# Kernel optimization log

Hardware: AMD Instinct MI355X
Metric: run time of the kernel (lower is better)

The kernel has to match this reference:

```python
import jax, jax.numpy as jnp
import numpy as np

EPS = 1e-12  # torch F.normalize default eps

def _l1_normalize(x):
    # F.normalize(x, p=1, dim=1): divide by channel-wise L1 norm, clamped at eps
    n = jnp.sum(jnp.abs(x), axis=1, keepdims=True)
    return x / jnp.maximum(n, EPS)

def setup_inputs() -> dict:
    key = jax.random.key(0)
    k1, k2, k3 = jax.random.split(key, 3)
    shape = (2, 128, 64, 64)  # B, C, H, W
    return {
        "a": jax.random.normal(k1, shape, dtype=jnp.float32),
        "b": jax.random.normal(k2, shape, dtype=jnp.float32),
        "c": jax.random.normal(k3, shape, dtype=jnp.float32),
    }

def reference(a, b, c):
    a = _l1_normalize(a)
    b = _l1_normalize(b)
    c = _l1_normalize(c)
    sim_ab = jnp.einsum('bchw,bcij->bhwij', a, b)
    sim_ac = jnp.einsum('bchw,bcij->bhwij', a, c)
    # F.l1_loss default reduction='mean'
    return jnp.mean(jnp.abs(sim_ac - sim_ab))
```

## Files before the change

### kernel.cpp

```cpp
#include <hip/hip_runtime.h>
#include <stdint.h>

#define HW 4096
#define NC 128
#define BATCH 2

typedef __attribute__((ext_vector_type(8))) short bf16x8;
typedef __attribute__((ext_vector_type(4))) float f32x4;
typedef __attribute__((ext_vector_type(8))) unsigned short u16x8;

__device__ __forceinline__ unsigned short f32_to_bf16(float f) {
    union { float f; unsigned int u; } v; v.f = f;
    unsigned int u = v.u;
    unsigned int r = (u + 0x7FFFu + ((u >> 16) & 1u)) >> 16;
    return (unsigned short)r;
}

__device__ __forceinline__ void async_cp16(const void* g, void* s) {
    __builtin_amdgcn_global_load_lds(
        (const __attribute__((address_space(1))) uint32_t*)g,
        (__attribute__((address_space(3))) uint32_t*)s, 16, 0, 0);
}

__global__ __launch_bounds__(512) void norm_kernel(
    const float* __restrict__ A, const float* __restrict__ B,
    const float* __restrict__ Cc,
    unsigned short* __restrict__ anT, unsigned short* __restrict__ dT,
    float* __restrict__ out) {
    const int tid = threadIdx.x;
    if (blockIdx.x == 0 && tid == 0) *out = 0.f;
    const int pl = tid & 31;
    const int cg = tid >> 5;
    const int gp = blockIdx.x * 32;
    const int bb = gp >> 12;
    const int p  = (gp & (HW - 1)) + pl;
    const size_t base = (size_t)bb * NC * HW + p;
    const int c0 = cg * 8;

    float va[8], vb[8], vc[8];
    float sa = 0.f, sb = 0.f, sc = 0.f;
#pragma unroll
    for (int k = 0; k < 8; ++k) {
        size_t idx = base + (size_t)(c0 + k) * HW;
        va[k] = A[idx]; vb[k] = B[idx]; vc[k] = Cc[idx];
        sa += fabsf(va[k]); sb += fabsf(vb[k]); sc += fabsf(vc[k]);
    }
    __shared__ float red[3][16][32];
    red[0][cg][pl] = sa; red[1][cg][pl] = sb; red[2][cg][pl] = sc;
    __syncthreads();
    float na = 0.f, nb = 0.f, nc = 0.f;
#pragma unroll
    for (int g = 0; g < 16; ++g) {
        na += red[0][g][pl]; nb += red[1][g][pl]; nc += red[2][g][pl];
    }
    const float ra = 1.f / fmaxf(na, 1e-12f);
    const float rb = 1.f / fmaxf(nb, 1e-12f);
    const float rc = 1.f / fmaxf(nc, 1e-12f);

    const size_t obase = ((size_t)bb * HW + p) * NC;
    const int slot = cg ^ (p & 15);
    u16x8 xa, xd;
#pragma unroll
    for (int j = 0; j < 8; ++j) {
        xa[j] = f32_to_bf16(va[j] * ra);
        xd[j] = f32_to_bf16(vc[j] * rc - vb[j] * rb);
    }
    *(u16x8*)(anT + obase + slot * 8) = xa;
    *(u16x8*)(dT  + obase + slot * 8) = xd;
}

__global__ __launch_bounds__(256, 2) void simloss_kernel(
    const unsigned short* __restrict__ anT, const unsigned short* __restrict__ dT,
    float* __restrict__ out) {
    __shared__ uint4 smem4[4096];
    const int tid = threadIdx.x;
    const int b   = blockIdx.x;
    const int bz  = b >> 8;
    const int my  = (b & 255) >> 3;
    const int ng  = b & 7;
    const char* gA = (const char*)(anT + ((size_t)bz * HW + my * 128) * NC);
    const char* gB0 = (const char*)(dT + ((size_t)bz * HW + ng * 4 * 128) * NC);

    const int wv  = tid >> 6;
    const int ln  = tid & 63;
    char* sA = (char*)smem4;
    char* sB = (char*)(smem4 + 2048);

#pragma unroll
    for (int i = 0; i < 8; ++i) {
        const size_t goff = (size_t)(i * 256 + tid) * 16;
        const size_t loff = (size_t)i * 4096 + wv * 1024;
        async_cp16(gA + goff, sA + loff);
        async_cp16(gB0 + goff, sB + loff);
    }
    __syncthreads();

    const int m16  = ln & 15;
    const int quad = ln >> 4;
    const int wr   = (wv >> 1) * 64;
    const int wc   = (wv & 1) * 64;

    float s = 0.f;
    for (int j = 0; j < 4; ++j) {
        f32x4 acc[4][4] = {};
#pragma unroll
        for (int ks = 0; ks < 4; ++ks) {
            const int chunk = ks * 4 + quad;
            const int slot  = chunk ^ m16;
            bf16x8 af[4], bfr[4];
#pragma unroll
            for (int mi = 0; mi < 4; ++mi)
                af[mi] = *(const bf16x8*)(sA + (wr + mi * 16 + m16) * 256 + slot * 16);
#pragma unroll
            for (int ni = 0; ni < 4; ++ni)
                bfr[ni] = *(const bf16x8*)(sB + (wc + ni * 16 + m16) * 256 + slot * 16);
#pragma unroll
            for (int mi = 0; mi < 4; ++mi)
#pragma unroll
                for (int ni = 0; ni < 4; ++ni)
                    acc[mi][ni] = __builtin_amdgcn_mfma_f32_16x16x32_bf16(
                        af[mi], bfr[ni], acc[mi][ni], 0, 0, 0);
        }
#pragma unroll
        for (int mi = 0; mi < 4; ++mi)
#pragma unroll
            for (int ni = 0; ni < 4; ++ni)
#pragma unroll
                for (int r = 0; r < 4; ++r)
                    s += fabsf(acc[mi][ni][r]);

        __syncthreads();
        if (j < 3) {
            const char* gBn = gB0 + (size_t)(j + 1) * 32768;
#pragma unroll
            for (int i = 0; i < 8; ++i) {
                const size_t goff = (size_t)(i * 256 + tid) * 16;
                const size_t loff = (size_t)i * 4096 + wv * 1024;
                async_cp16(gBn + goff, sB + loff);
            }
            __syncthreads();
        }
    }

#pragma unroll
    for (int off = 32; off > 0; off >>= 1)
        s += __shfl_down(s, off);
    if (ln == 0) ((float*)smem4)[wv] = s;
    __syncthreads();
    if (tid == 0) {
        const float inv = 1.0f / ((float)BATCH * (float)HW * (float)HW);
        float t = ((float*)smem4)[0] + ((float*)smem4)[1] +
                  ((float*)smem4)[2] + ((float*)smem4)[3];
        atomicAdd(out, t * inv);
    }
}

extern "C" void kernel_launch(void* const* d_in, const int* in_sizes, int n_in,
                              void* d_out, int out_size, void* d_ws, size_t ws_size,
                              hipStream_t stream) {
    const float* A  = (const float*)d_in[0];
    const float* B  = (const float*)d_in[1];
    const float* Cc = (const float*)d_in[2];
    float* out = (float*)d_out;
    unsigned short* anT = (unsigned short*)d_ws;
    unsigned short* dT  = anT + (size_t)BATCH * HW * NC;

    norm_kernel<<<dim3(256), dim3(512), 0, stream>>>(A, B, Cc, anT, dT, out);
    simloss_kernel<<<dim3(512), dim3(256), 0, stream>>>(anT, dT, out);
}
```

Before: 79.90 us.

## Keep A fragments in registers and double-buffer B tiles in LDS

The similarity kernel now loads its A-tile MFMA fragments into registers once. That frees the A region of shared memory to act as a second B buffer, so the next B tile's async global-to-LDS copy runs while the current tile is being computed, and one barrier per iteration is removed. The normalization kernel is also reshaped so each thread handles two pixels with float2 loads, using 256 threads per block instead of 512. The cost is higher register pressure from the 64 VGPRs of A fragments, which could limit occupancy under the existing launch bounds.

After: 80.73 us. No clear change (+1.0%).

```diff
diff --git a/kernel.cpp b/kernel.cpp
--- a/kernel.cpp
+++ b/kernel.cpp
@@ -22,51 +22,65 @@
         (__attribute__((address_space(3))) uint32_t*)s, 16, 0, 0);
 }
 
-__global__ __launch_bounds__(512) void norm_kernel(
+__global__ __launch_bounds__(256) void norm_kernel(
     const float* __restrict__ A, const float* __restrict__ B,
     const float* __restrict__ Cc,
     unsigned short* __restrict__ anT, unsigned short* __restrict__ dT,
     float* __restrict__ out) {
     const int tid = threadIdx.x;
     if (blockIdx.x == 0 && tid == 0) *out = 0.f;
-    const int pl = tid & 31;
-    const int cg = tid >> 5;
+    const int pl = tid & 15;
+    const int cg = tid >> 4;
     const int gp = blockIdx.x * 32;
     const int bb = gp >> 12;
-    const int p  = (gp & (HW - 1)) + pl;
-    const size_t base = (size_t)bb * NC * HW + p;
+    const int p0 = (gp & (HW - 1)) + pl * 2;
+    const size_t base = (size_t)bb * NC * HW + p0;
     const int c0 = cg * 8;
 
-    float va[8], vb[8], vc[8];
-    float sa = 0.f, sb = 0.f, sc = 0.f;
+    float2 va[8], vb[8], vc[8];
+    float sa0 = 0.f, sa1 = 0.f, sb0 = 0.f, sb1 = 0.f, sc0 = 0.f, sc1 = 0.f;
 #pragma unroll
     for (int k = 0; k < 8; ++k) {
         size_t idx = base + (size_t)(c0 + k) * HW;
-        va[k] = A[idx]; vb[k] = B[idx]; vc[k] = Cc[idx];
-        sa += fabsf(va[k]); sb += fabsf(vb[k]); sc += fabsf(vc[k]);
+        va[k] = *(const float2*)(A + idx);
+        vb[k] = *(const float2*)(B + idx);
+        vc[k] = *(const float2*)(Cc + idx);
+        sa0 += fabsf(va[k].x); sa1 += fabsf(va[k].y);
+        sb0 += fabsf(vb[k].x); sb1 += fabsf(vb[k].y);
+        sc0 += fabsf(vc[k].x); sc1 += fabsf(vc[k].y);
     }
     __shared__ float red[3][16][32];
-    red[0][cg][pl] = sa; red[1][cg][pl] = sb; red[2][cg][pl] = sc;
+    red[0][cg][pl * 2] = sa0; red[0][cg][pl * 2 + 1] = sa1;
+    red[1][cg][pl * 2] = sb0; red[1][cg][pl * 2 + 1] = sb1;
+    red[2][cg][pl * 2] = sc0; red[2][cg][pl * 2 + 1] = sc1;
     __syncthreads();
-    float na = 0.f, nb = 0.f, nc = 0.f;
+    float na0 = 0.f, na1 = 0.f, nb0 = 0.f, nb1 = 0.f, nc0 = 0.f, nc1 = 0.f;
 #pragma unroll
     for (int g = 0; g < 16; ++g) {
-        na += red[0][g][pl]; nb += red[1][g][pl]; nc += red[2][g][pl];
+        na0 += red[0][g][pl * 2]; na1 += red[0][g][pl * 2 + 1];
+        nb0 += red[1][g][pl * 2]; nb1 += red[1][g][pl * 2 + 1];
+        nc0 += red[2][g][pl * 2]; nc1 += red[2][g][pl * 2 + 1];
     }
-    const float ra = 1.f / fmaxf(na, 1e-12f);
-    const float rb = 1.f / fmaxf(nb, 1e-12f);
-    const float rc = 1.f / fmaxf(nc, 1e-12f);
+    const float ra0 = 1.f / fmaxf(na0, 1e-12f), ra1 = 1.f / fmaxf(na1, 1e-12f);
+    const float rb0 = 1.f / fmaxf(nb0, 1e-12f), rb1 = 1.f / fmaxf(nb1, 1e-12f);
+    const float rc0 = 1.f / fmaxf(nc0, 1e-12f), rc1 = 1.f / fmaxf(nc1, 1e-12f);
 
-    const size_t obase = ((size_t)bb * HW + p) * NC;
-    const int slot = cg ^ (p & 15);
-    u16x8 xa, xd;
+    const size_t ob0 = ((size_t)bb * HW + p0) * NC;
+    const size_t ob1 = ob0 + NC;
+    const int sl0 = cg ^ (p0 & 15);
+    const int sl1 = cg ^ ((p0 + 1) & 15);
+    u16x8 xa0, xa1, xd0, xd1;
 #pragma unroll
     for (int j = 0; j < 8; ++j) {
-        xa[j] = f32_to_bf16(va[j] * ra);
-        xd[j] = f32_to_bf16(vc[j] * rc - vb[j] * rb);
+        xa0[j] = f32_to_bf16(va[j].x * ra0);
+        xa1[j] = f32_to_bf16(va[j].y * ra1);
+        xd0[j] = f32_to_bf16(vc[j].x * rc0 - vb[j].x * rb0);
+        xd1[j] = f32_to_bf16(vc[j].y * rc1 - vb[j].y * rb1);
     }
-    *(u16x8*)(anT + obase + slot * 8) = xa;
-    *(u16x8*)(dT  + obase + slot * 8) = xd;
+    *(u16x8*)(anT + ob0 + sl0 * 8) = xa0;
+    *(u16x8*)(anT + ob1 + sl1 * 8) = xa1;
+    *(u16x8*)(dT  + ob0 + sl0 * 8) = xd0;
+    *(u16x8*)(dT  + ob1 + sl1 * 8) = xd1;
 }
 
 __global__ __launch_bounds__(256, 2) void simloss_kernel(
@@ -78,20 +92,20 @@
     const int bz  = b >> 8;
     const int my  = (b & 255) >> 3;
     const int ng  = b & 7;
-    const char* gA = (const char*)(anT + ((size_t)bz * HW + my * 128) * NC);
+    const char* gA  = (const char*)(anT + ((size_t)bz * HW + my * 128) * NC);
     const char* gB0 = (const char*)(dT + ((size_t)bz * HW + ng * 4 * 128) * NC);
 
-    const int wv  = tid >> 6;
-    const int ln  = tid & 63;
-    char* sA = (char*)smem4;
-    char* sB = (char*)(smem4 + 2048);
+    const int wv = tid >> 6;
+    const int ln = tid & 63;
+    char* buf0 = (char*)smem4;
+    char* buf1 = (char*)(smem4 + 2048);
 
 #pragma unroll
     for (int i = 0; i < 8; ++i) {
         const size_t goff = (size_t)(i * 256 + tid) * 16;
         const size_t loff = (size_t)i * 4096 + wv * 1024;
-        async_cp16(gA + goff, sA + loff);
-        async_cp16(gB0 + goff, sB + loff);
+        async_cp16(gA + goff, buf0 + loff);
+        async_cp16(gB0 + goff, buf1 + loff);
     }
     __syncthreads();
 
@@ -100,17 +114,40 @@
     const int wr   = (wv >> 1) * 64;
     const int wc   = (wv & 1) * 64;
 
+    bf16x8 aF[4][4];
+#pragma unroll
+    for (int ks = 0; ks < 4; ++ks) {
+        const int slot = (ks * 4 + quad) ^ m16;
+#pragma unroll
+        for (int mi = 0; mi < 4; ++mi)
+            aF[mi][ks] = *(const bf16x8*)(buf0 + (wr + mi * 16 + m16) * 256 + slot * 16);
+    }
+    __syncthreads();
+
+#pragma unroll
+    for (int i = 0; i < 8; ++i)
+        async_cp16(gB0 + 32768 + (size_t)(i * 256 + tid) * 16,
+                   buf0 + (size_t)i * 4096 + wv * 1024);
+
     float s = 0.f;
     for (int j = 0; j < 4; ++j) {
+        if (j) {
+            __syncthreads();
+            if (j < 3) {
+                char* dst = (j & 1) ? buf1 : buf0;
+                const char* src = gB0 + (size_t)(j + 1) * 32768;
+#pragma unroll
+                for (int i = 0; i < 8; ++i)
+                    async_cp16(src + (size_t)(i * 256 + tid) * 16,
+                               dst + (size_t)i * 4096 + wv * 1024);
+            }
+        }
+        const char* sB = (j & 1) ? buf0 : buf1;
         f32x4 acc[4][4] = {};
 #pragma unroll
         for (int ks = 0; ks < 4; ++ks) {
-            const int chunk = ks * 4 + quad;
-            const int slot  = chunk ^ m16;
-            bf16x8 af[4], bfr[4];
-#pragma unroll
-            for (int mi = 0; mi < 4; ++mi)
-                af[mi] = *(const bf16x8*)(sA + (wr + mi * 16 + m16) * 256 + slot * 16);
+            const int slot = (ks * 4 + quad) ^ m16;
+            bf16x8 bfr[4];
 #pragma unroll
             for (int ni = 0; ni < 4; ++ni)
                 bfr[ni] = *(const bf16x8*)(sB + (wc + ni * 16 + m16) * 256 + slot * 16);
@@ -119,7 +156,7 @@
 #pragma unroll
                 for (int ni = 0; ni < 4; ++ni)
                     acc[mi][ni] = __builtin_amdgcn_mfma_f32_16x16x32_bf16(
-                        af[mi], bfr[ni], acc[mi][ni], 0, 0, 0);
+                        aF[mi][ks], bfr[ni], acc[mi][ni], 0, 0, 0);
         }
 #pragma unroll
         for (int mi = 0; mi < 4; ++mi)
@@ -128,23 +165,12 @@
 #pragma unroll
                 for (int r = 0; r < 4; ++r)
                     s += fabsf(acc[mi][ni][r]);
-
-        __syncthreads();
-        if (j < 3) {
-            const char* gBn = gB0 + (size_t)(j + 1) * 32768;
-#pragma unroll
-            for (int i = 0; i < 8; ++i) {
-                const size_t goff = (size_t)(i * 256 + tid) * 16;
-                const size_t loff = (size_t)i * 4096 + wv * 1024;
-                async_cp16(gBn + goff, sB + loff);
-            }
-            __syncthreads();
-        }
     }
 
 #pragma unroll
     for (int off = 32; off > 0; off >>= 1)
         s += __shfl_down(s, off);
+    __syncthreads();
     if (ln == 0) ((float*)smem4)[wv] = s;
     __syncthreads();
     if (tid == 0) {
@@ -165,6 +191,6 @@
     unsigned short* anT = (unsigned short*)d_ws;
     unsigned short* dT  = anT + (size_t)BATCH * HW * NC;
 
-    norm_kernel<<<dim3(256), dim3(512), 0, stream>>>(A, B, Cc, anT, dT, out);
+    norm_kernel<<<dim3(256), dim3(256), 0, stream>>>(A, B, Cc, anT, dT, out);
     simloss_kernel<<<dim3(512), dim3(256), 0, stream>>>(anT, dT, out);
 }
```
